# Kernel optimization log

Hardware: AMD Instinct MI355X
Metric: run time of the kernel (lower is better)

The kernel has to match this reference:

```python
import jax, jax.numpy as jnp
import numpy as np

N_PAD, N_PAS = 14, 8
N_H = 2 + N_PAD            # 16
MHID, RN, NINF = 256, 256, 256
N_NODES, N_EDGES, N_GRAPHS = 40000, 640000, 64


def _dense_params(key, fin, fout):
    w = jax.random.normal(key, (fin, fout), jnp.float32) / np.float32(np.sqrt(fin))
    return w, jnp.zeros((fout,), jnp.float32)


def setup_inputs() -> dict:
    key = jax.random.key(0)
    ks = jax.random.split(key, 17)
    x = jax.random.normal(ks[0], (N_NODES, 2), jnp.float32)
    e = jax.random.normal(ks[1], (N_EDGES, 1), jnp.float32)
    first = jax.random.randint(ks[2], (N_EDGES,), 0, N_NODES, jnp.int32)
    second = jax.random.randint(ks[3], (N_EDGES,), 0, N_NODES, jnp.int32)
    segment = jnp.sort(jax.random.randint(ks[4], (N_NODES,), 0, N_GRAPHS, jnp.int32))
    l_w1, l_b1 = _dense_params(ks[5], 1, MHID)
    l_w2, l_b2 = _dense_params(ks[6], MHID, N_H * N_H)
    b_w1, b_b1 = _dense_params(ks[7], 1, MHID)
    b_w2, b_b2 = _dense_params(ks[8], MHID, N_H)
    gru_k = jax.random.normal(ks[9], (N_H, 3 * N_H), jnp.float32) / np.float32(np.sqrt(N_H))
    gru_rk = jax.random.normal(ks[10], (N_H, 3 * N_H), jnp.float32) / np.float32(np.sqrt(N_H))
    gru_b = jnp.zeros((2, 3 * N_H), jnp.float32)  # [input_bias, recurrent_bias] (reset_after=True)
    i_w1, i_b1 = _dense_params(ks[11], N_H + 2, RN)
    i_w2, i_b2 = _dense_params(ks[12], RN, RN)
    j_w1, j_b1 = _dense_params(ks[13], N_H + 2, RN)
    j_w2, j_b2 = _dense_params(ks[14], RN, RN)
    f_w1, f_b1 = _dense_params(ks[15], RN, NINF)
    f_w2, f_b2 = _dense_params(ks[16], NINF, 1)
    return dict(x=x, e=e, first=first, second=second, segment=segment,
                l_w1=l_w1, l_b1=l_b1, l_w2=l_w2, l_b2=l_b2,
                b_w1=b_w1, b_b1=b_b1, b_w2=b_w2, b_b2=b_b2,
                gru_k=gru_k, gru_rk=gru_rk, gru_b=gru_b,
                i_w1=i_w1, i_b1=i_b1, i_w2=i_w2, i_b2=i_b2,
                j_w1=j_w1, j_b1=j_b1, j_w2=j_w2, j_b2=j_b2,
                f_w1=f_w1, f_b1=f_b1, f_w2=f_w2, f_b2=f_b2)


def reference(x, e, first, second, segment,
              l_w1, l_b1, l_w2, l_b2,
              b_w1, b_b1, b_w2, b_b2,
              gru_k, gru_rk, gru_b,
              i_w1, i_b1, i_w2, i_b2,
              j_w1, j_b1, j_w2, j_b2,
              f_w1, f_b1, f_w2, f_b2):
    selu = jax.nn.selu
    # Edge-conditioned message weights depend only on e; identical across passes, so hoist.
    a = (selu(e @ l_w1 + l_b1) @ l_w2 + l_b2).reshape(-1, N_H, N_H)  # [E, N_H, N_H]
    bvec = selu(e @ b_w1 + b_b1) @ b_w2 + b_b2                       # [E, N_H]
    h = jnp.pad(x, ((0, 0), (0, N_PAD)))                             # [N, N_H]
    for _ in range(N_PAS):
        m = jnp.einsum('eij,ej->ei', a, h[first]) + bvec             # per-edge matmul + bias
        m = jax.ops.segment_sum(m, second, num_segments=N_NODES)     # scatter-add to nodes
        # Keras GRUCell (reset_after=True)
        mx = m @ gru_k + gru_b[0]
        mh = h @ gru_rk + gru_b[1]
        xz, xr, xh = jnp.split(mx, 3, axis=1)
        rz, rr, rh = jnp.split(mh, 3, axis=1)
        z = jax.nn.sigmoid(xz + rz)
        r = jax.nn.sigmoid(xr + rr)
        hh = jnp.tanh(xh + r * rh)
        h = z * h + (1.0 - z) * hh
    # Readout R: gated sum over nodes of each graph (segment sorted)
    hx = jnp.concatenate([h, x], axis=1)                             # [N, N_H+2]
    gate = jax.nn.sigmoid(jnp.tanh(hx @ i_w1 + i_b1) @ i_w2 + i_b2)  # [N, RN]
    feat = selu(hx @ j_w1 + j_b1) @ j_w2 + j_b2                      # [N, RN]
    node_batch = jax.ops.segment_sum(gate * feat, segment, num_segments=N_GRAPHS)
    return selu(node_batch @ f_w1 + f_b1) @ f_w2 + f_b2              # [G, 1]
```

## Files before the change

### kernel.cpp

```cpp
#include <hip/hip_runtime.h>

#define E_EDGES 640000
#define N_NODES 40000
#define NGRAPH  64
#define TPTS    2048
#define TMIN    -6.0f
#define TSPAN   12.0f
#define NBLK    157
#define SBLK    256
#define EPB     2500
#define EPB2    128

typedef _Float16 h16x8 __attribute__((ext_vector_type(8)));
typedef float f32x4 __attribute__((ext_vector_type(4)));

__device__ __forceinline__ f32x4 mfma16h(h16x8 a, h16x8 b, f32x4 c) {
    return __builtin_amdgcn_mfma_f32_16x16x32_f16(a, b, c, 0, 0, 0);
}
__device__ __forceinline__ unsigned short f2h(float f) {
    union { _Float16 h; unsigned short u; } v; v.h = (_Float16)f; return v.u;
}
__device__ __forceinline__ float selu_f(float v) {
    const float sc = 1.0507009873554805f;
    const float sa = 1.7580993408473766f;
    return v > 0.f ? sc * v : sa * (__expf(v) - 1.f);
}
__device__ __forceinline__ float sigm_f(float v) { return 1.f / (1.f + __expf(-v)); }
__device__ __forceinline__ float tanh_f(float v) { return 2.f / (1.f + __expf(-2.f * v)) - 1.f; }
__device__ __forceinline__ void tcoord(float t, int& g, float& fr) {
    float tt = (t - TMIN) * ((float)(TPTS - 1) / TSPAN);
    tt = fminf(fmaxf(tt, 0.f), (float)(TPTS - 1));
    int gi = (int)tt;
    if (gi > TPTS - 2) gi = TPTS - 2;
    g = gi; fr = tt - (float)gi;
}

__global__ void k_zero_out(float* __restrict__ out, int n) {
    int i = blockIdx.x * 64 + threadIdx.x;
    if (i < n) out[i] = 0.f;
}

__global__ __launch_bounds__(256) void k_init(const float* __restrict__ x,
                                              float* __restrict__ h0,
                                              int* __restrict__ counts) {
    int idx = blockIdx.x * 256 + threadIdx.x;
    if (idx < N_NODES * 16) {
        int j = idx & 15, n = idx >> 4;
        h0[idx] = (j < 2) ? x[n * 2 + j] : 0.f;
    }
    if (idx < N_NODES) counts[idx] = 0;
}

__global__ __launch_bounds__(256) void k_count(const int* __restrict__ second,
                                               int* __restrict__ counts) {
    int e = blockIdx.x * 256 + threadIdx.x;
    if (e < E_EDGES) atomicAdd(&counts[second[e]], 1);
}

__global__ __launch_bounds__(256) void k_scanA(const int* __restrict__ counts,
                                               int* __restrict__ offs,
                                               int* __restrict__ bsum) {
    __shared__ int lds[256];
    int tid = threadIdx.x;
    int base = blockIdx.x * 256;
    int v = (base + tid < N_NODES) ? counts[base + tid] : 0;
    lds[tid] = v;
    __syncthreads();
    for (int d = 1; d < 256; d <<= 1) {
        int t2 = (tid >= d) ? lds[tid - d] : 0;
        __syncthreads();
        lds[tid] += t2;
        __syncthreads();
    }
    if (base + tid < N_NODES) offs[base + tid] = lds[tid] - v;
    if (tid == 255) bsum[blockIdx.x] = lds[255];
}

__global__ __launch_bounds__(256) void k_scanB(const int* __restrict__ bsum,
                                               int* __restrict__ boff) {
    __shared__ int lds[256];
    int tid = threadIdx.x;
    int v = (tid < NBLK) ? bsum[tid] : 0;
    lds[tid] = v;
    __syncthreads();
    for (int d = 1; d < 256; d <<= 1) {
        int t2 = (tid >= d) ? lds[tid - d] : 0;
        __syncthreads();
        lds[tid] += t2;
        __syncthreads();
    }
    if (tid < NBLK) boff[tid] = lds[tid] - v;
}

__global__ __launch_bounds__(256) void k_scanC(int* __restrict__ offs,
                                               int* __restrict__ cur,
                                               const int* __restrict__ boff) {
    int tid = threadIdx.x;
    int i = blockIdx.x * 256 + tid;
    if (i < N_NODES) {
        int o = offs[i] + boff[blockIdx.x];
        offs[i] = o;
        cur[i] = o;
    }
    if (i == 0) offs[N_NODES] = E_EDGES;
}

__global__ __launch_bounds__(256) void k_scatter(const int* __restrict__ second,
                                                 const int* __restrict__ first,
                                                 const float* __restrict__ e,
                                                 int* __restrict__ cur,
                                                 int* __restrict__ fs,
                                                 float* __restrict__ ev) {
    int i = blockIdx.x * 256 + threadIdx.x;
    if (i < E_EDGES) {
        int pos = atomicAdd(&cur[second[i]], 1);
        fs[pos] = first[i];
        ev[pos] = e[i];
    }
}

__global__ __launch_bounds__(256) void k_hist(const float* __restrict__ ev,
                                              int* __restrict__ histG) {
    __shared__ int hcnt[TPTS];
    int tid = threadIdx.x, b = blockIdx.x;
    for (int c = tid; c < TPTS; c += 256) hcnt[c] = 0;
    __syncthreads();
    int s = b * EPB;
    for (int it = 0; it < 10; ++it) {
        int p = s + it * 256 + tid;
        if (p < s + EPB) {
            int g; float fr;
            tcoord(ev[p], g, fr);
            atomicAdd(&hcnt[g], 1);
        }
    }
    __syncthreads();
    for (int c = tid; c < TPTS; c += 256) histG[c * SBLK + b] = hcnt[c];
}

__global__ __launch_bounds__(256) void k_gscanA(const int* __restrict__ in,
                                                int* __restrict__ out,
                                                int* __restrict__ bsum) {
    __shared__ int lds[256];
    int tid = threadIdx.x;
    int base = blockIdx.x * 256;
    int v = in[base + tid];
    lds[tid] = v;
    __syncthreads();
    for (int d = 1; d < 256; d <<= 1) {
        int t2 = (tid >= d) ? lds[tid - d] : 0;
        __syncthreads();
        lds[tid] += t2;
        __syncthreads();
    }
    out[base + tid] = lds[tid] - v;
    if (tid == 255) bsum[blockIdx.x] = lds[255];
}

__global__ __launch_bounds__(256) void k_scan2(const int* __restrict__ in,
                                               int* __restrict__ out) {
    __shared__ int lds[256];
    __shared__ int carry;
    int tid = threadIdx.x;
    if (tid == 0) carry = 0;
    __syncthreads();
    for (int base = 0; base < TPTS; base += 256) {
        int v = in[base + tid];
        lds[tid] = v;
        __syncthreads();
        for (int d = 1; d < 256; d <<= 1) {
            int t2 = (tid >= d) ? lds[tid - d] : 0;
            __syncthreads();
            lds[tid] += t2;
            __syncthreads();
        }
        int incl = lds[tid];
        int c0 = carry;
        out[base + tid] = c0 + incl - v;
        __syncthreads();
        if (tid == 255) carry = c0 + incl;
        __syncthreads();
    }
}

__global__ __launch_bounds__(256) void k_gscanC(int* __restrict__ out,
                                                const int* __restrict__ boff) {
    out[blockIdx.x * 256 + threadIdx.x] += boff[blockIdx.x];
}

__global__ __launch_bounds__(256) void k_sort(
    const int* __restrict__ fs, const float* __restrict__ ev,
    const int* __restrict__ baseG, int4* __restrict__ spk) {
    __shared__ int hcnt[TPTS];
    int tid = threadIdx.x, b = blockIdx.x;
    for (int c = tid; c < TPTS; c += 256) hcnt[c] = 0;
    __syncthreads();
    int s = b * EPB;
    for (int it = 0; it < 10; ++it) {
        int p = s + it * 256 + tid;
        if (p < s + EPB) {
            float e = ev[p];
            int g; float fr;
            tcoord(e, g, fr);
            int r = atomicAdd(&hcnt[g], 1);
            int q = baseG[g * SBLK + b] + r;
            spk[q] = make_int4(fs[p], __float_as_int(e), p, 0);
        }
    }
}

__global__ __launch_bounds__(256) void k_tab(
    const float* __restrict__ lw1, const float* __restrict__ lb1,
    const float* __restrict__ lw2, const float* __restrict__ lb2,
    const float* __restrict__ bw1, const float* __restrict__ bb1,
    const float* __restrict__ bw2, const float* __restrict__ bb2,
    float* __restrict__ ta, float* __restrict__ tb) {
    __shared__ float hl[256];
    __shared__ float hb[256];
    int tid = threadIdx.x;
    int g = blockIdx.x;
    const float STEP = TSPAN / (float)(TPTS - 1);
    float t = TMIN + (float)g * STEP;
    hl[tid] = selu_f(t * lw1[tid] + lb1[tid]);
    hb[tid] = selu_f(t * bw1[tid] + bb1[tid]);
    __syncthreads();
    float acc = 0.f, accB = 0.f;
    for (int k = 0; k < 256; ++k) {
        float w = lw2[k * 256 + tid];
        float wb = (tid < 16) ? bw2[k * 16 + tid] : 0.f;
        acc += hl[k] * w;
        accB += hb[k] * wb;
    }
    ta[g * 256 + tid] = acc + lb2[tid];
    if (tid < 16) tb[g * 16 + tid] = accB + bb2[tid];
}

__global__ __launch_bounds__(256) void k_w2prep(const float* __restrict__ iw2,
                                                const float* __restrict__ jw2,
                                                unsigned short* __restrict__ iw2t,
                                                unsigned short* __restrict__ jw2t) {
    int idx = blockIdx.x * 256 + threadIdx.x;
    int k = idx >> 8, n = idx & 255;
    iw2t[n * 256 + k] = f2h(iw2[idx]);
    jw2t[n * 256 + k] = f2h(jw2[idx]);
}

__global__ __launch_bounds__(256) void k_bvnode(const float* __restrict__ tb,
                                                const int* __restrict__ offs,
                                                const float* __restrict__ ev,
                                                float* __restrict__ bvn) {
    int idx = blockIdx.x * 256 + threadIdx.x;
    int node = idx >> 4, i = idx & 15;
    int beg = offs[node], end = offs[node + 1];
    float s = 0.f;
    for (int p = beg; p < end; ++p) {
        int g; float fr;
        tcoord(ev[p], g, fr);
        float v0 = tb[g * 16 + i], v1 = tb[g * 16 + 16 + i];
        s += v0 + fr * (v1 - v0);
    }
    bvn[idx] = s;
}

__global__ __launch_bounds__(256) void k_msg2(
    const float* __restrict__ ta, const int4* __restrict__ spk,
    const float* __restrict__ hin, float* __restrict__ msg) {
    const int tid = threadIdx.x;
    const int i = tid & 15;
    int q = blockIdx.x * EPB2 + (tid >> 4);
    int gcur = -1;
    float4 a0 = {0, 0, 0, 0}, a1 = a0, a2 = a0, a3 = a0;
    float4 c0 = a0, c1 = a0, c2 = a0, c3 = a0;
    int4 pA = spk[q];
    int4 pB = spk[q + 16];
    const float4* hpA = (const float4*)(hin + pA.x * 16);
    float4 hA0 = hpA[0], hA1 = hpA[1], hA2 = hpA[2], hA3 = hpA[3];
    const float4* hpB = (const float4*)(hin + pB.x * 16);
    float4 hB0 = hpB[0], hB1 = hpB[1], hB2 = hpB[2], hB3 = hpB[3];
    const int PITERS = EPB2 / 32;
    for (int it = 0; it < PITERS; ++it) {
        int4 nA = pA, nB = pB;
        float4 mA0 = {0,0,0,0}, mA1 = mA0, mA2 = mA0, mA3 = mA0;
        float4 mB0 = mA0, mB1 = mA0, mB2 = mA0, mB3 = mA0;
        if (it + 1 < PITERS) {
            nA = spk[q + 32];
            nB = spk[q + 48];
            const float4* ha = (const float4*)(hin + nA.x * 16);
            mA0 = ha[0]; mA1 = ha[1]; mA2 = ha[2]; mA3 = ha[3];
            const float4* hbp = (const float4*)(hin + nB.x * 16);
            mB0 = hbp[0]; mB1 = hbp[1]; mB2 = hbp[2]; mB3 = hbp[3];
        }
        {
            int g; float fr;
            tcoord(__int_as_float(pA.y), g, fr);
            if (g != gcur) {
                gcur = g;
                const float4* A0 = (const float4*)(ta + g * 256 + i * 16);
                a0 = A0[0]; a1 = A0[1]; a2 = A0[2]; a3 = A0[3];
                c0 = A0[64]; c1 = A0[65]; c2 = A0[66]; c3 = A0[67];
            }
            float da = a0.x * hA0.x + a0.y * hA0.y + a0.z * hA0.z + a0.w * hA0.w
                     + a1.x * hA1.x + a1.y * hA1.y + a1.z * hA1.z + a1.w * hA1.w
                     + a2.x * hA2.x + a2.y * hA2.y + a2.z * hA2.z + a2.w * hA2.w
                     + a3.x * hA3.x + a3.y * hA3.y + a3.z * hA3.z + a3.w * hA3.w;
            float dc = c0.x * hA0.x + c0.y * hA0.y + c0.z * hA0.z + c0.w * hA0.w
                     + c1.x * hA1.x + c1.y * hA1.y + c1.z * hA1.z + c1.w * hA1.w
                     + c2.x * hA2.x + c2.y * hA2.y + c2.z * hA2.z + c2.w * hA2.w
                     + c3.x * hA3.x + c3.y * hA3.y + c3.z * hA3.z + c3.w * hA3.w;
            msg[pA.z * 16 + i] = da + fr * (dc - da);
        }
        {
            int g; float fr;
            tcoord(__int_as_float(pB.y), g, fr);
            if (g != gcur) {
                gcur = g;
                const float4* A0 = (const float4*)(ta + g * 256 + i * 16);
                a0 = A0[0]; a1 = A0[1]; a2 = A0[2]; a3 = A0[3];
                c0 = A0[64]; c1 = A0[65]; c2 = A0[66]; c3 = A0[67];
            }
            float da = a0.x * hB0.x + a0.y * hB0.y + a0.z * hB0.z + a0.w * hB0.w
                     + a1.x * hB1.x + a1.y * hB1.y + a1.z * hB1.z + a1.w * hB1.w
                     + a2.x * hB2.x + a2.y * hB2.y + a2.z * hB2.z + a2.w * hB2.w
                     + a3.x * hB3.x + a3.y * hB3.y + a3.z * hB3.z + a3.w * hB3.w;
            float dc = c0.x * hB0.x + c0.y * hB0.y + c0.z * hB0.z + c0.w * hB0.w
                     + c1.x * hB1.x + c1.y * hB1.y + c1.z * hB1.z + c1.w * hB1.w
                     + c2.x * hB2.x + c2.y * hB2.y + c2.z * hB2.z + c2.w * hB2.w
                     + c3.x * hB3.x + c3.y * hB3.y + c3.z * hB3.z + c3.w * hB3.w;
            msg[pB.z * 16 + i] = da + fr * (dc - da);
        }
        q += 32;
        pA = nA; pB = nB;
        hA0 = mA0; hA1 = mA1; hA2 = mA2; hA3 = mA3;
        hB0 = mB0; hB1 = mB1; hB2 = mB2; hB3 = mB3;
    }
}

__global__ __launch_bounds__(256) void k_gru(
    const float* __restrict__ msg, const float* __restrict__ bvn,
    const int* __restrict__ offs,
    const float* __restrict__ hin, float* __restrict__ hout,
    const float* __restrict__ gk, const float* __restrict__ grk,
    const float* __restrict__ gb) {
    __shared__ float l_gk[768], l_grk[768], l_gb[96];
    int tid = threadIdx.x;
    for (int i2 = tid; i2 < 768; i2 += 256) { l_gk[i2] = gk[i2]; l_grk[i2] = grk[i2]; }
    if (tid < 96) l_gb[tid] = gb[tid];
    __syncthreads();

    int idx = blockIdx.x * 256 + tid;
    int node = idx >> 4, i = idx & 15;
    int lane = tid & 63, lbase = lane & ~15;
    int beg = offs[node], end = offs[node + 1];
    float acc = bvn[idx];
    for (int p = beg; p < end; ++p) acc += msg[p * 16 + i];

    float mxz = l_gb[i], mxr = l_gb[16 + i], mxh = l_gb[32 + i];
    float mhz = l_gb[48 + i], mhr = l_gb[64 + i], mhh = l_gb[80 + i];
    const float* hrow = hin + node * 16;
#pragma unroll
    for (int j = 0; j < 16; ++j) {
        float mj = __shfl(acc, lbase + j);
        float hj = hrow[j];
        mxz += mj * l_gk[j * 48 + i];       mhz += hj * l_grk[j * 48 + i];
        mxr += mj * l_gk[j * 48 + 16 + i];  mhr += hj * l_grk[j * 48 + 16 + i];
        mxh += mj * l_gk[j * 48 + 32 + i];  mhh += hj * l_grk[j * 48 + 32 + i];
    }
    float z = sigm_f(mxz + mhz);
    float r = sigm_f(mxr + mhr);
    float hh = tanh_f(mxh + r * mhh);
    float hi = hrow[i];
    hout[idx] = z * hi + (1.f - z) * hh;
}

__global__ __launch_bounds__(256) void k_ro1(
    const float* __restrict__ h, const float* __restrict__ x,
    const float* __restrict__ iw1, const float* __restrict__ ib1,
    const float* __restrict__ jw1, const float* __restrict__ jb1,
    unsigned short* __restrict__ ui, unsigned short* __restrict__ uj,
    float* __restrict__ nb) {
    __shared__ float w_i[18 * 256];
    __shared__ float w_j[18 * 256];
    __shared__ float hx[32][18];
    int tid = threadIdx.x;
    int nb0 = blockIdx.x * 32;
    if (blockIdx.x < NGRAPH) nb[blockIdx.x * 256 + tid] = 0.f;
    for (int idx = tid; idx < 18 * 256; idx += 256) {
        w_i[idx] = iw1[idx];
        w_j[idx] = jw1[idx];
    }
    for (int idx = tid; idx < 32 * 18; idx += 256) {
        int nl = idx / 18, k = idx - nl * 18;
        hx[nl][k] = (k < 16) ? h[(nb0 + nl) * 16 + k] : x[(nb0 + nl) * 2 + (k - 16)];
    }
    __syncthreads();
    float bi = ib1[tid], bj = jb1[tid];
    for (int nl = 0; nl < 32; ++nl) {
        float ai = bi, aj = bj;
#pragma unroll
        for (int k = 0; k < 18; ++k) {
            float hv = hx[nl][k];
            ai += hv * w_i[k * 256 + tid];
            aj += hv * w_j[k * 256 + tid];
        }
        ui[(size_t)(nb0 + nl) * 256 + tid] = f2h(tanh_f(ai));
        uj[(size_t)(nb0 + nl) * 256 + tid] = f2h(selu_f(aj));
    }
}

__global__ __launch_bounds__(256) void k_ro23(
    const unsigned short* __restrict__ ui, const unsigned short* __restrict__ uj,
    const unsigned short* __restrict__ iw2t, const float* __restrict__ ib2,
    const unsigned short* __restrict__ jw2t, const float* __restrict__ jb2,
    const int* __restrict__ seg, float* __restrict__ nb) {
    __shared__ alignas(16) unsigned short ldsBg[64 * 40];
    __shared__ alignas(16) unsigned short ldsBf[64 * 40];
    const int tid = threadIdx.x;
    const int cq = blockIdx.x;
    const int w = tid >> 6, lane = tid & 63;
    const int m = lane & 15, quad = lane >> 4;
    const int rowBase = blockIdx.y * 64 + w * 16;
    const int rowA = rowBase + m;
    const int col0 = cq * 64;

    f32x4 accg[4], accf[4];
#pragma unroll
    for (int nt = 0; nt < 4; ++nt) {
        accg[nt] = (f32x4){0.f, 0.f, 0.f, 0.f};
        accf[nt] = (f32x4){0.f, 0.f, 0.f, 0.f};
    }

    const int col_l = tid >> 2;
    const int koff = (tid & 3) * 8;
    for (int kc = 0; kc < 8; ++kc) {
        __syncthreads();
        {
            const unsigned short* sg = iw2t + (col0 + col_l) * 256 + kc * 32 + koff;
            const unsigned short* sf = jw2t + (col0 + col_l) * 256 + kc * 32 + koff;
            uint4 vg = *(const uint4*)sg;
            uint4 vf = *(const uint4*)sf;
            *(uint4*)&ldsBg[col_l * 40 + koff] = vg;
            *(uint4*)&ldsBf[col_l * 40 + koff] = vf;
        }
        __syncthreads();
        const int kk = kc * 32 + quad * 8;
        h16x8 ag = *(const h16x8*)&ui[(size_t)rowA * 256 + kk];
        h16x8 af = *(const h16x8*)&uj[(size_t)rowA * 256 + kk];
        const unsigned short* bpg = &ldsBg[m * 40 + quad * 8];
        const unsigned short* bpf = &ldsBf[m * 40 + quad * 8];
#pragma unroll
        for (int nt = 0; nt < 4; ++nt) {
            h16x8 bg = *(const h16x8*)(bpg + nt * 640);
            h16x8 bf = *(const h16x8*)(bpf + nt * 640);
            accg[nt] = mfma16h(ag, bg, accg[nt]);
            accf[nt] = mfma16h(af, bf, accf[nt]);
        }
    }

    const int s_lo = seg[rowBase], s_hi = seg[rowBase + 15];
    if (s_lo == s_hi) {
#pragma unroll
        for (int nt = 0; nt < 4; ++nt) {
            int col = col0 + nt * 16 + m;
            float bi = ib2[col], bj = jb2[col];
            float vr = 0.f;
#pragma unroll
            for (int reg = 0; reg < 4; ++reg) {
                float g = sigm_f(accg[nt][reg] + bi);
                float f = accf[nt][reg] + bj;
                vr += g * f;
            }
            vr += __shfl_xor(vr, 16);
            vr += __shfl_xor(vr, 32);
            if (quad == 0) atomicAdd(&nb[s_lo * 256 + col], vr);
        }
    } else {
#pragma unroll
        for (int nt = 0; nt < 4; ++nt) {
            int col = col0 + nt * 16 + m;
            float bi = ib2[col], bj = jb2[col];
            int cur = seg[rowBase + quad * 4];
            float sum = 0.f;
#pragma unroll
            for (int reg = 0; reg < 4; ++reg) {
                int s = seg[rowBase + quad * 4 + reg];
                float g = sigm_f(accg[nt][reg] + bi);
                float f = accf[nt][reg] + bj;
                if (s != cur) { atomicAdd(&nb[cur * 256 + col], sum); cur = s; sum = 0.f; }
                sum += g * f;
            }
            atomicAdd(&nb[cur * 256 + col], sum);
        }
    }
}

__global__ __launch_bounds__(256) void k_final(const float* __restrict__ nb,
                                               const float* __restrict__ fw1,
                                               const float* __restrict__ fb1,
                                               const float* __restrict__ fw2,
                                               const float* __restrict__ fb2,
                                               float* __restrict__ out) {
    __shared__ float red[4];
    int t = threadIdx.x, g = blockIdx.x;
    float acc = fb1[t];
    for (int k = 0; k < 256; ++k) acc += nb[g * 256 + k] * fw1[k * 256 + t];
    float v = selu_f(acc) * fw2[t];
#pragma unroll
    for (int off = 32; off > 0; off >>= 1) v += __shfl_down(v, off);
    if ((t & 63) == 0) red[t >> 6] = v;
    __syncthreads();
    if (t == 0) out[g] = red[0] + red[1] + red[2] + red[3] + fb2[0];
}

extern "C" void kernel_launch(void* const* d_in, const int* in_sizes, int n_in,
                              void* d_out, int out_size, void* d_ws, size_t ws_size,
                              hipStream_t stream) {
    const float* x    = (const float*)d_in[0];
    const float* e    = (const float*)d_in[1];
    const int* first  = (const int*)d_in[2];
    const int* second = (const int*)d_in[3];
    const int* seg    = (const int*)d_in[4];
    const float* lw1  = (const float*)d_in[5];
    const float* lb1  = (const float*)d_in[6];
    const float* lw2  = (const float*)d_in[7];
    const float* lb2  = (const float*)d_in[8];
    const float* bw1  = (const float*)d_in[9];
    const float* bb1  = (const float*)d_in[10];
    const float* bw2  = (const float*)d_in[11];
    const float* bb2  = (const float*)d_in[12];
    const float* gk   = (const float*)d_in[13];
    const float* grk  = (const float*)d_in[14];
    const float* gb   = (const float*)d_in[15];
    const float* iw1  = (const float*)d_in[16];
    const float* ib1  = (const float*)d_in[17];
    const float* iw2  = (const float*)d_in[18];
    const float* ib2  = (const float*)d_in[19];
    const float* jw1  = (const float*)d_in[20];
    const float* jb1  = (const float*)d_in[21];
    const float* jw2  = (const float*)d_in[22];
    const float* jb2  = (const float*)d_in[23];
    const float* fw1  = (const float*)d_in[24];
    const float* fb1  = (const float*)d_in[25];
    const float* fw2  = (const float*)d_in[26];
    const float* fb2  = (const float*)d_in[27];
    (void)in_sizes; (void)n_in;

    float* OUT = (float*)d_out;

    const size_t REQ = 153168896ULL;
    if (ws_size < REQ) {
        k_zero_out<<<(out_size + 63) / 64, 64, 0, stream>>>(OUT, out_size);
        return;
    }

    char* ws = (char*)d_ws;
    float* TA   = (float*)(ws + 0);
    float* TB   = (float*)(ws + 2097152);
    float* H0   = (float*)(ws + 2228224);
    float* H1   = (float*)(ws + 4788224);
    float* BVN  = (float*)(ws + 7348224);
    int* CNT    = (int*)(ws + 9908224);
    int* OFF    = (int*)(ws + 10068224);
    int* CUR    = (int*)(ws + 10228480);
    int* BSUM   = (int*)(ws + 10388480);
    int* BOFF   = (int*)(ws + 10389504);
    int* FS     = (int*)(ws + 10390528);
    float* EV   = (float*)(ws + 12950528);
    int* HIST   = (int*)(ws + 15510528);
    int* BASE   = (int*)(ws + 17607680);
    int* BSUM2  = (int*)(ws + 19704832);
    int* BOFF2  = (int*)(ws + 19713024);
    int4* SPK   = (int4*)(ws + 19721216);
    char* ro    = ws + 29961216;
    float* MSG  = (float*)(ro + 0);
    unsigned short* UI = (unsigned short*)(ro + 0);
    unsigned short* UJ = (unsigned short*)(ro + 20480000);
    float* NB   = (float*)(ro + 122880000);
    unsigned short* IW2T = (unsigned short*)(ro + 122945536);
    unsigned short* JW2T = (unsigned short*)(ro + 123076608);

    k_init<<<2500, 256, 0, stream>>>(x, H0, CNT);
    k_count<<<2500, 256, 0, stream>>>(second, CNT);
    k_scanA<<<NBLK, 256, 0, stream>>>(CNT, OFF, BSUM);
    k_scanB<<<1, 256, 0, stream>>>(BSUM, BOFF);
    k_scanC<<<NBLK, 256, 0, stream>>>(OFF, CUR, BOFF);
    k_scatter<<<2500, 256, 0, stream>>>(second, first, e, CUR, FS, EV);
    k_hist<<<SBLK, 256, 0, stream>>>(EV, HIST);
    k_gscanA<<<TPTS * SBLK / 256, 256, 0, stream>>>(HIST, BASE, BSUM2);
    k_scan2<<<1, 256, 0, stream>>>(BSUM2, BOFF2);
    k_gscanC<<<TPTS * SBLK / 256, 256, 0, stream>>>(BASE, BOFF2);
    k_sort<<<SBLK, 256, 0, stream>>>(FS, EV, BASE, SPK);
    k_tab<<<TPTS, 256, 0, stream>>>(lw1, lb1, lw2, lb2, bw1, bb1, bw2, bb2, TA, TB);
    k_w2prep<<<256, 256, 0, stream>>>(iw2, jw2, IW2T, JW2T);
    k_bvnode<<<2500, 256, 0, stream>>>(TB, OFF, EV, BVN);
    const float* hin = H0;
    float* hout = H1;
    for (int p = 0; p < 8; ++p) {
        k_msg2<<<E_EDGES / EPB2, 256, 0, stream>>>(TA, SPK, hin, MSG);
        k_gru<<<2500, 256, 0, stream>>>(MSG, BVN, OFF, hin, hout, gk, grk, gb);
        const float* t = hout; hout = (float*)hin; hin = t;
    }
    k_ro1<<<1250, 256, 0, stream>>>(hin, x, iw1, ib1, jw1, jb1, UI, UJ, NB);
    k_ro23<<<dim3(4, 625), 256, 0, stream>>>(UI, UJ, IW2T, ib2, JW2T, jb2, seg, NB);
    k_final<<<64, 256, 0, stream>>>(NB, fw1, fb1, fw2, fb2, OUT);
}
```

Measured before the change: 870.7 us.

## Drop CSR scatter and per-node bias kernel; sort edges directly from inputs

The CSR scatter that copied first/e into node-sorted order is replaced by a kernel that only records each edge's CSR position, and the table-sort kernel now reads first and e straight from the inputs. The per-node bias precompute (k_bvnode) is removed. Its interpolated bias term is instead added to each edge's message inside k_msg2, so the GRU kernel no longer reads a bias buffer. This cuts two passes over edge data and one kernel in setup, at the cost of two extra table loads and a few FLOPs per edge in each of the 8 message passes.

```diff
diff --git a/kernel.cpp b/kernel.cpp
--- a/kernel.cpp
+++ b/kernel.cpp
@@ -105,21 +105,14 @@
     if (i == 0) offs[N_NODES] = E_EDGES;
 }
 
-__global__ __launch_bounds__(256) void k_scatter(const int* __restrict__ second,
-                                                 const int* __restrict__ first,
-                                                 const float* __restrict__ e,
-                                                 int* __restrict__ cur,
-                                                 int* __restrict__ fs,
-                                                 float* __restrict__ ev) {
+__global__ __launch_bounds__(256) void k_epos(const int* __restrict__ second,
+                                              int* __restrict__ cur,
+                                              int* __restrict__ epos) {
     int i = blockIdx.x * 256 + threadIdx.x;
-    if (i < E_EDGES) {
-        int pos = atomicAdd(&cur[second[i]], 1);
-        fs[pos] = first[i];
-        ev[pos] = e[i];
-    }
-}
-
-__global__ __launch_bounds__(256) void k_hist(const float* __restrict__ ev,
+    if (i < E_EDGES) epos[i] = atomicAdd(&cur[second[i]], 1);
+}
+
+__global__ __launch_bounds__(256) void k_hist(const float* __restrict__ e,
                                               int* __restrict__ histG) {
     __shared__ int hcnt[TPTS];
     int tid = threadIdx.x, b = blockIdx.x;
@@ -130,7 +123,7 @@
         int p = s + it * 256 + tid;
         if (p < s + EPB) {
             int g; float fr;
-            tcoord(ev[p], g, fr);
+            tcoord(e[p], g, fr);
             atomicAdd(&hcnt[g], 1);
         }
     }
@@ -189,8 +182,9 @@
 }
 
 __global__ __launch_bounds__(256) void k_sort(
-    const int* __restrict__ fs, const float* __restrict__ ev,
-    const int* __restrict__ baseG, int4* __restrict__ spk) {
+    const int* __restrict__ first, const float* __restrict__ e,
+    const int* __restrict__ epos, const int* __restrict__ baseG,
+    int4* __restrict__ spk) {
     __shared__ int hcnt[TPTS];
     int tid = threadIdx.x, b = blockIdx.x;
     for (int c = tid; c < TPTS; c += 256) hcnt[c] = 0;
@@ -199,12 +193,12 @@
     for (int it = 0; it < 10; ++it) {
         int p = s + it * 256 + tid;
         if (p < s + EPB) {
-            float e = ev[p];
+            float ee = e[p];
             int g; float fr;
-            tcoord(e, g, fr);
+            tcoord(ee, g, fr);
             int r = atomicAdd(&hcnt[g], 1);
             int q = baseG[g * SBLK + b] + r;
-            spk[q] = make_int4(fs[p], __float_as_int(e), p, 0);
+            spk[q] = make_int4(first[p], __float_as_int(ee), epos[p], 0);
         }
     }
 }
@@ -245,25 +239,9 @@
     jw2t[n * 256 + k] = f2h(jw2[idx]);
 }
 
-__global__ __launch_bounds__(256) void k_bvnode(const float* __restrict__ tb,
-                                                const int* __restrict__ offs,
-                                                const float* __restrict__ ev,
-                                                float* __restrict__ bvn) {
-    int idx = blockIdx.x * 256 + threadIdx.x;
-    int node = idx >> 4, i = idx & 15;
-    int beg = offs[node], end = offs[node + 1];
-    float s = 0.f;
-    for (int p = beg; p < end; ++p) {
-        int g; float fr;
-        tcoord(ev[p], g, fr);
-        float v0 = tb[g * 16 + i], v1 = tb[g * 16 + 16 + i];
-        s += v0 + fr * (v1 - v0);
-    }
-    bvn[idx] = s;
-}
-
 __global__ __launch_bounds__(256) void k_msg2(
-    const float* __restrict__ ta, const int4* __restrict__ spk,
+    const float* __restrict__ ta, const float* __restrict__ tb,
+    const int4* __restrict__ spk,
     const float* __restrict__ hin, float* __restrict__ msg) {
     const int tid = threadIdx.x;
     const int i = tid & 15;
@@ -271,6 +249,7 @@
     int gcur = -1;
     float4 a0 = {0, 0, 0, 0}, a1 = a0, a2 = a0, a3 = a0;
     float4 c0 = a0, c1 = a0, c2 = a0, c3 = a0;
+    float tba = 0.f, tbc = 0.f;
     int4 pA = spk[q];
     int4 pB = spk[q + 16];
     const float4* hpA = (const float4*)(hin + pA.x * 16);
@@ -298,6 +277,8 @@
                 const float4* A0 = (const float4*)(ta + g * 256 + i * 16);
                 a0 = A0[0]; a1 = A0[1]; a2 = A0[2]; a3 = A0[3];
                 c0 = A0[64]; c1 = A0[65]; c2 = A0[66]; c3 = A0[67];
+                tba = tb[g * 16 + i];
+                tbc = tb[g * 16 + 16 + i];
             }
             float da = a0.x * hA0.x + a0.y * hA0.y + a0.z * hA0.z + a0.w * hA0.w
                      + a1.x * hA1.x + a1.y * hA1.y + a1.z * hA1.z + a1.w * hA1.w
@@ -307,7 +288,7 @@
                      + c1.x * hA1.x + c1.y * hA1.y + c1.z * hA1.z + c1.w * hA1.w
                      + c2.x * hA2.x + c2.y * hA2.y + c2.z * hA2.z + c2.w * hA2.w
                      + c3.x * hA3.x + c3.y * hA3.y + c3.z * hA3.z + c3.w * hA3.w;
-            msg[pA.z * 16 + i] = da + fr * (dc - da);
+            msg[pA.z * 16 + i] = da + fr * (dc - da) + tba + fr * (tbc - tba);
         }
         {
             int g; float fr;
@@ -317,6 +298,8 @@
                 const float4* A0 = (const float4*)(ta + g * 256 + i * 16);
                 a0 = A0[0]; a1 = A0[1]; a2 = A0[2]; a3 = A0[3];
                 c0 = A0[64]; c1 = A0[65]; c2 = A0[66]; c3 = A0[67];
+                tba = tb[g * 16 + i];
+                tbc = tb[g * 16 + 16 + i];
             }
             float da = a0.x * hB0.x + a0.y * hB0.y + a0.z * hB0.z + a0.w * hB0.w
                      + a1.x * hB1.x + a1.y * hB1.y + a1.z * hB1.z + a1.w * hB1.w
@@ -326,7 +309,7 @@
                      + c1.x * hB1.x + c1.y * hB1.y + c1.z * hB1.z + c1.w * hB1.w
                      + c2.x * hB2.x + c2.y * hB2.y + c2.z * hB2.z + c2.w * hB2.w
                      + c3.x * hB3.x + c3.y * hB3.y + c3.z * hB3.z + c3.w * hB3.w;
-            msg[pB.z * 16 + i] = da + fr * (dc - da);
+            msg[pB.z * 16 + i] = da + fr * (dc - da) + tba + fr * (tbc - tba);
         }
         q += 32;
         pA = nA; pB = nB;
@@ -336,8 +319,7 @@
 }
 
 __global__ __launch_bounds__(256) void k_gru(
-    const float* __restrict__ msg, const float* __restrict__ bvn,
-    const int* __restrict__ offs,
+    const float* __restrict__ msg, const int* __restrict__ offs,
     const float* __restrict__ hin, float* __restrict__ hout,
     const float* __restrict__ gk, const float* __restrict__ grk,
     const float* __restrict__ gb) {
@@ -351,7 +333,7 @@
     int node = idx >> 4, i = idx & 15;
     int lane = tid & 63, lbase = lane & ~15;
     int beg = offs[node], end = offs[node + 1];
-    float acc = bvn[idx];
+    float acc = 0.f;
     for (int p = beg; p < end; ++p) acc += msg[p * 16 + i];
 
     float mxz = l_gb[i], mxr = l_gb[16 + i], mxh = l_gb[32 + i];
@@ -546,7 +528,7 @@
 
     float* OUT = (float*)d_out;
 
-    const size_t REQ = 153168896ULL;
+    const size_t REQ = 148048896ULL;
     if (ws_size < REQ) {
         k_zero_out<<<(out_size + 63) / 64, 64, 0, stream>>>(OUT, out_size);
         return;
@@ -557,20 +539,18 @@
     float* TB   = (float*)(ws + 2097152);
     float* H0   = (float*)(ws + 2228224);
     float* H1   = (float*)(ws + 4788224);
-    float* BVN  = (float*)(ws + 7348224);
-    int* CNT    = (int*)(ws + 9908224);
-    int* OFF    = (int*)(ws + 10068224);
-    int* CUR    = (int*)(ws + 10228480);
-    int* BSUM   = (int*)(ws + 10388480);
-    int* BOFF   = (int*)(ws + 10389504);
-    int* FS     = (int*)(ws + 10390528);
-    float* EV   = (float*)(ws + 12950528);
-    int* HIST   = (int*)(ws + 15510528);
-    int* BASE   = (int*)(ws + 17607680);
-    int* BSUM2  = (int*)(ws + 19704832);
-    int* BOFF2  = (int*)(ws + 19713024);
-    int4* SPK   = (int4*)(ws + 19721216);
-    char* ro    = ws + 29961216;
+    int* CNT    = (int*)(ws + 7348224);
+    int* OFF    = (int*)(ws + 7508224);
+    int* CUR    = (int*)(ws + 7668480);
+    int* BSUM   = (int*)(ws + 7828480);
+    int* BOFF   = (int*)(ws + 7829504);
+    int* EPOS   = (int*)(ws + 7830528);
+    int* HIST   = (int*)(ws + 10390528);
+    int* BASE   = (int*)(ws + 12487680);
+    int* BSUM2  = (int*)(ws + 14584832);
+    int* BOFF2  = (int*)(ws + 14593024);
+    int4* SPK   = (int4*)(ws + 14601216);
+    char* ro    = ws + 24841216;
     float* MSG  = (float*)(ro + 0);
     unsigned short* UI = (unsigned short*)(ro + 0);
     unsigned short* UJ = (unsigned short*)(ro + 20480000);
@@ -583,20 +563,19 @@
     k_scanA<<<NBLK, 256, 0, stream>>>(CNT, OFF, BSUM);
     k_scanB<<<1, 256, 0, stream>>>(BSUM, BOFF);
     k_scanC<<<NBLK, 256, 0, stream>>>(OFF, CUR, BOFF);
-    k_scatter<<<2500, 256, 0, stream>>>(second, first, e, CUR, FS, EV);
-    k_hist<<<SBLK, 256, 0, stream>>>(EV, HIST);
+    k_epos<<<2500, 256, 0, stream>>>(second, CUR, EPOS);
+    k_hist<<<SBLK, 256, 0, stream>>>(e, HIST);
     k_gscanA<<<TPTS * SBLK / 256, 256, 0, stream>>>(HIST, BASE, BSUM2);
     k_scan2<<<1, 256, 0, stream>>>(BSUM2, BOFF2);
     k_gscanC<<<TPTS * SBLK / 256, 256, 0, stream>>>(BASE, BOFF2);
-    k_sort<<<SBLK, 256, 0, stream>>>(FS, EV, BASE, SPK);
+    k_sort<<<SBLK, 256, 0, stream>>>(first, e, EPOS, BASE, SPK);
     k_tab<<<TPTS, 256, 0, stream>>>(lw1, lb1, lw2, lb2, bw1, bb1, bw2, bb2, TA, TB);
     k_w2prep<<<256, 256, 0, stream>>>(iw2, jw2, IW2T, JW2T);
-    k_bvnode<<<2500, 256, 0, stream>>>(TB, OFF, EV, BVN);
     const float* hin = H0;
     float* hout = H1;
     for (int p = 0; p < 8; ++p) {
-        k_msg2<<<E_EDGES / EPB2, 256, 0, stream>>>(TA, SPK, hin, MSG);
-        k_gru<<<2500, 256, 0, stream>>>(MSG, BVN, OFF, hin, hout, gk, grk, gb);
+        k_msg2<<<E_EDGES / EPB2, 256, 0, stream>>>(TA, TB, SPK, hin, MSG);
+        k_gru<<<2500, 256, 0, stream>>>(MSG, OFF, hin, hout, gk, grk, gb);
         const float* t = hout; hout = (float*)hin; hin = t;
     }
     k_ro1<<<1250, 256, 0, stream>>>(hin, x, iw1, ib1, jw1, jb1, UI, UJ, NB);
```

Result: faster. 848.3 us, median of 2 (-2.6%).
